# Kernel tuning notes

Measured on AMD Instinct MI355X. Metric: run time of the kernel, lower is better.

The kernel has to match this reference:

```python
import jax, jax.numpy as jnp
import numpy as np

B, C, D, H, W = 4, 128, 16, 16, 16
P = 64  # proj_dim (spatial branch is dead code in the original fusion; params omitted)


def setup_inputs() -> dict:
    key = jax.random.key(0)
    ks = jax.random.split(key, 10)
    lin = lambda k, o, i: 0.02 * jax.random.normal(k, (o, i), jnp.float32)
    return {
        "x": jax.random.normal(ks[0], (B, C, D, H, W), jnp.float32),
        "ln_g": jnp.ones((C,), jnp.float32),
        "ln_b": jnp.zeros((C,), jnp.float32),
        "Wq": lin(ks[1], C, C), "bq": jnp.zeros((C,), jnp.float32),
        "Wk": lin(ks[2], C, C), "bk": jnp.zeros((C,), jnp.float32),
        "Wvc": lin(ks[3], C, C), "bvc": jnp.zeros((C,), jnp.float32),
        "Wvch": lin(ks[4], C, C), "bvch": jnp.zeros((C,), jnp.float32),
        "Wconv": 0.02 * jax.random.normal(ks[5], (2, C, 3, 3, 3), jnp.float32),
        "bconv": jnp.zeros((2,), jnp.float32),
        "Wg": lin(ks[6], 3, C), "bg": jnp.zeros((3,), jnp.float32),
    }


def reference(x, ln_g, ln_b, Wq, bq, Wk, bk, Wvc, bvc, Wvch, bvch, Wconv, bconv, Wg, bg):
    b, c, d, h, w = x.shape
    n = d * h * w
    # LayerNorm over channels (permute to channels-last)
    xp = jnp.transpose(x, (0, 2, 3, 4, 1))                      # (B,D,H,W,C)
    mu = jnp.mean(xp, axis=-1, keepdims=True)
    var = jnp.mean((xp - mu) ** 2, axis=-1, keepdims=True)
    xn = (xp - mu) * jax.lax.rsqrt(var + 1e-5) * ln_g + ln_b     # (B,D,H,W,C)
    x_norm = jnp.transpose(xn, (0, 4, 1, 2, 3))                  # (B,C,D,H,W)
    # Causal Growth Field prediction: Conv3d C->2, k=3, SAME padding
    cgf = jax.lax.conv_general_dilated(
        x_norm, Wconv, (1, 1, 1), "SAME",
        dimension_numbers=("NCDHW", "OIDHW", "NCDHW")) + bconv[None, :, None, None, None]
    # Token sequence (B,N,C); same flattening order as x_norm.view(B,C,-1).transpose(1,2)
    xf = xn.reshape(b, n, c)
    q = jnp.einsum("bnc,oc->bno", xf, Wq) + bq
    k = jnp.einsum("bnc,oc->bno", xf, Wk) + bk
    # --- causal branch: full NxN attention ---
    vc = jnp.einsum("bnc,oc->bno", xf, Wvc) + bvc
    attn_causal = jax.nn.softmax(jnp.einsum("bnc,bmc->bnm", q, k) / (c ** 0.5), axis=-1)
    out_causal = jnp.einsum("bnm,bmc->bnc", attn_causal, vc)
    # --- channel branch: CxC attention ---
    vch = jnp.einsum("bnc,oc->bno", xf, Wvch) + bvch
    attn_channel = jax.nn.softmax(jnp.einsum("bnc,bnd->bcd", q, k) / (n ** 0.5), axis=-1)
    out_channel = jnp.einsum("bcd,bnd->bnc", attn_channel, vch)
    # --- gated fusion (original uses only weights 0 and 2; spatial branch is dead code) ---
    pooled = jnp.mean(x, axis=(2, 3, 4))                          # (B,C)
    weights = jax.nn.softmax(pooled @ Wg.T + bg, axis=-1)         # (B,3)
    fused = (weights[:, 0][:, None, None] * out_causal
             + weights[:, 2][:, None, None] * out_channel)        # (B,N,C)
    output = x + jnp.transpose(fused, (0, 2, 1)).reshape(b, c, d, h, w)
    return (output, cgf)
```

## Files before the change

kernel.cpp:

```cpp
#include <hip/hip_runtime.h>
#include <math.h>

#define CH   128
#define NSP  4096
#define BATCH 4
#define BIG  (BATCH*NSP*CH)
#define KCHUNKS 64
#define FKSPLIT 4
#define MB (1024*1024)

typedef short short8 __attribute__((ext_vector_type(8)));
typedef float floatx4 __attribute__((ext_vector_type(4)));

__device__ __forceinline__ unsigned short f2bu(float f) {
  union { float f; unsigned u; } v; v.f = f;
  unsigned r = v.u + 0x7fffu + ((v.u >> 16) & 1u);
  return (unsigned short)(r >> 16);
}
__device__ __forceinline__ float b2f(unsigned short h) {
  union { unsigned u; float f; } v; v.u = ((unsigned)h) << 16;
  return v.f;
}

__global__ __launch_bounds__(256) void ln_kernel(const float* __restrict__ x,
    const float* __restrict__ g, const float* __restrict__ bta,
    unsigned short* __restrict__ xfb) {
  __shared__ float tile[128][65];
  __shared__ float pS[4][64];
  __shared__ float pQ[4][64];
  __shared__ float mu_s[64], rs_s[64];
  int t = threadIdx.x;
  int b  = blockIdx.x >> 6;
  int n0 = (blockIdx.x & 63) << 6;
  for (int i = t; i < 8192; i += 256) {
    int c = i >> 6, n = i & 63;
    tile[c][n] = x[(size_t)(b*CH + c)*NSP + n0 + n];
  }
  __syncthreads();
  {
    int n = t & 63, part = t >> 6;
    float s = 0.f, qq = 0.f;
    for (int c = part; c < 128; c += 4) { float v = tile[c][n]; s += v; qq += v*v; }
    pS[part][n] = s; pQ[part][n] = qq;
  }
  __syncthreads();
  if (t < 64) {
    float s = pS[0][t] + pS[1][t] + pS[2][t] + pS[3][t];
    float qq = pQ[0][t] + pQ[1][t] + pQ[2][t] + pQ[3][t];
    float mu = s * (1.f/128.f);
    float var = qq * (1.f/128.f) - mu*mu;
    mu_s[t] = mu;
    rs_s[t] = rsqrtf(var + 1e-5f);
  }
  __syncthreads();
  for (int i = t; i < 8192; i += 256) {
    int n = i >> 7, c = i & 127;
    float v = (tile[c][n] - mu_s[n]) * rs_s[n] * g[c] + bta[c];
    xfb[(size_t)(b*NSP + n0 + n)*CH + c] = f2bu(v);
  }
}

__global__ __launch_bounds__(256) void pooled_kernel(const float* __restrict__ x,
                                                     float* __restrict__ pooled) {
  int bc = blockIdx.x; int t = threadIdx.x;
  const float4* p = (const float4*)(x + (size_t)bc*NSP);
  float s = 0.f;
  for (int i = t; i < 1024; i += 256) { float4 v = p[i]; s += v.x+v.y+v.z+v.w; }
  for (int off = 32; off; off >>= 1) s += __shfl_xor(s, off, 64);
  __shared__ float red[4];
  if ((t & 63) == 0) red[t >> 6] = s;
  __syncthreads();
  if (t == 0) pooled[bc] = (red[0]+red[1]+red[2]+red[3]) * (1.f/4096.f);
}

__global__ void gate_kernel(const float* __restrict__ pooled, const float* __restrict__ Wg,
                            const float* __restrict__ bg, float* __restrict__ wgt) {
  __shared__ float lg[4][3];
  int t = threadIdx.x;
  if (t < 12) {
    int b = t / 3, j = t % 3;
    float s = bg[j];
    const float* pr = pooled + b*CH;
    const float* wr = Wg + j*CH;
    for (int c = 0; c < CH; ++c) s += pr[c]*wr[c];
    lg[b][j] = s;
  }
  __syncthreads();
  if (t < 4) {
    float a = lg[t][0], b2 = lg[t][1], c = lg[t][2];
    float m = fmaxf(a, fmaxf(b2, c));
    float e0 = __expf(a-m), e1 = __expf(b2-m), e2 = __expf(c-m);
    float inv = 1.f/(e0+e1+e2);
    wgt[t*3+0] = e0*inv; wgt[t*3+1] = e1*inv; wgt[t*3+2] = e2*inv;
  }
}

__global__ __launch_bounds__(256) void conv_kernel(const unsigned short* __restrict__ xfb,
    const float* __restrict__ Wc, const float* __restrict__ bc_, float* __restrict__ cgf) {
  __shared__ float Wl[27*256];
  int t = threadIdx.x;
  for (int i = t; i < 6912; i += 256) {
    int tap = i >> 8;
    int rem = i & 255;
    int o = rem >> 7, c = rem & 127;
    Wl[i] = Wc[o*3456 + c*27 + tap];
  }
  __syncthreads();
  int cg = t & 15, spl = t >> 4;
  int sp = blockIdx.x*16 + spl;
  int b = sp >> 12, n = sp & 4095;
  int z = n >> 8, y = (n >> 4) & 15, xw = n & 15;
  const unsigned short* xb = xfb + (size_t)b*NSP*CH + cg*8;
  float a0 = 0.f, a1 = 0.f;
  for (int kd = 0; kd < 3; ++kd) {
    int zz = z + kd - 1; if ((unsigned)zz >= 16u) continue;
    for (int kh = 0; kh < 3; ++kh) {
      int yy = y + kh - 1; if ((unsigned)yy >= 16u) continue;
      #pragma unroll
      for (int kw = 0; kw < 3; ++kw) {
        int xx = xw + kw - 1; if ((unsigned)xx >= 16u) continue;
        int nn = (zz << 8) + (yy << 4) + xx;
        short8 xv = *(const short8*)(xb + (size_t)nn*CH);
        int tap = (kd*3 + kh)*3 + kw;
        const float* wbase = &Wl[tap*256 + cg*8];
        float4 w00 = *(const float4*)(wbase);
        float4 w01 = *(const float4*)(wbase + 4);
        float4 w10 = *(const float4*)(wbase + 128);
        float4 w11 = *(const float4*)(wbase + 132);
        float x0 = b2f((unsigned short)xv[0]), x1 = b2f((unsigned short)xv[1]);
        float x2 = b2f((unsigned short)xv[2]), x3 = b2f((unsigned short)xv[3]);
        float x4 = b2f((unsigned short)xv[4]), x5 = b2f((unsigned short)xv[5]);
        float x6 = b2f((unsigned short)xv[6]), x7 = b2f((unsigned short)xv[7]);
        a0 += x0*w00.x + x1*w00.y + x2*w00.z + x3*w00.w
            + x4*w01.x + x5*w01.y + x6*w01.z + x7*w01.w;
        a1 += x0*w10.x + x1*w10.y + x2*w10.z + x3*w10.w
            + x4*w11.x + x5*w11.y + x6*w11.z + x7*w11.w;
      }
    }
  }
  #pragma unroll
  for (int off = 1; off <= 8; off <<= 1) {
    a0 += __shfl_xor(a0, off, 64);
    a1 += __shfl_xor(a1, off, 64);
  }
  if (cg == 0) {
    cgf[b*8192 + n]        = a0 + bc_[0];
    cgf[b*8192 + 4096 + n] = a1 + bc_[1];
  }
}

__global__ __launch_bounds__(256) void wcast_kernel(const float* __restrict__ Wq,
    const float* __restrict__ Wk, const float* __restrict__ Wvc,
    const float* __restrict__ Wvch, unsigned short* __restrict__ Wb) {
  int idx = blockIdx.x*256 + threadIdx.x;
  int pj = idx >> 14, wi = idx & 16383;
  const float* src = (pj == 0) ? Wq : (pj == 1) ? Wk : (pj == 2) ? Wvc : Wvch;
  Wb[idx] = f2bu(src[wi]);
}

__global__ __launch_bounds__(256) void proj_mfma_kernel(
    const unsigned short* __restrict__ xfb, const unsigned short* __restrict__ Wb,
    const float* __restrict__ bq, const float* __restrict__ bk,
    const float* __restrict__ bvc, const float* __restrict__ bvch,
    unsigned short* __restrict__ q, unsigned short* __restrict__ k,
    unsigned short* __restrict__ vc, unsigned short* __restrict__ vch) {
  __shared__ __align__(16) unsigned short Ws[128][136];
  int t = threadIdx.x;
  int lane = t & 63, w = t >> 6;
  int id = lane & 15, quad = lane >> 4;
  int pj = blockIdx.y;
  int r0 = blockIdx.x*128 + w*32;

  const unsigned short* Wp = Wb + ((size_t)pj << 14);
  for (int i = t; i < 2048; i += 256) {
    int rr = i >> 4, c8 = (i & 15) << 3;
    *(short8*)&Ws[rr][c8] = *(const short8*)(Wp + rr*CH + c8);
  }
  short8 af[2][4];
  #pragma unroll
  for (int m = 0; m < 2; ++m)
    #pragma unroll
    for (int kc = 0; kc < 4; ++kc)
      af[m][kc] = *(const short8*)(xfb + (size_t)(r0 + m*16 + id)*CH + kc*32 + quad*8);
  __syncthreads();

  floatx4 acc[2][8];
  #pragma unroll
  for (int m = 0; m < 2; ++m)
    #pragma unroll
    for (int nt = 0; nt < 8; ++nt) acc[m][nt] = (floatx4){0.f,0.f,0.f,0.f};
  #pragma unroll
  for (int nt = 0; nt < 8; ++nt)
    #pragma unroll
    for (int kc = 0; kc < 4; ++kc) {
      short8 bf = *(const short8*)&Ws[nt*16 + id][kc*32 + quad*8];
      acc[0][nt] = __builtin_amdgcn_mfma_f32_16x16x32_bf16(af[0][kc], bf, acc[0][nt], 0, 0, 0);
      acc[1][nt] = __builtin_amdgcn_mfma_f32_16x16x32_bf16(af[1][kc], bf, acc[1][nt], 0, 0, 0);
    }

  const float* bias = (pj == 0) ? bq : (pj == 1) ? bk : (pj == 2) ? bvc : bvch;
  unsigned short* Y = (pj == 0) ? q : (pj == 1) ? k : (pj == 2) ? vc : vch;
  #pragma unroll
  for (int nt = 0; nt < 8; ++nt) {
    float bsv = bias[nt*16 + id];
    #pragma unroll
    for (int m = 0; m < 2; ++m)
      #pragma unroll
      for (int r = 0; r < 4; ++r) {
        int row = r0 + m*16 + quad*4 + r;
        Y[(size_t)row*CH + nt*16 + id] = f2bu(acc[m][nt][r] + bsv);
      }
  }
}

__global__ __launch_bounds__(256) void vtrans_kernel(const unsigned short* __restrict__ vc,
                                                     unsigned short* __restrict__ vct) {
  __shared__ unsigned short T[128][72];
  int t = threadIdx.x;
  int b = blockIdx.x >> 6, n0 = (blockIdx.x & 63) << 6;
  for (int i = t; i < 1024; i += 256) {
    int n = i >> 4, c0 = (i & 15) << 3;
    short8 v = *(const short8*)&vc[(size_t)(b*NSP + n0 + n)*CH + c0];
    #pragma unroll
    for (int j = 0; j < 8; ++j) T[c0+j][n] = (unsigned short)v[j];
  }
  __syncthreads();
  for (int i = t; i < 1024; i += 256) {
    int c = i >> 3, k8 = (i & 7) << 3;
    *(short8*)&vct[((size_t)b*CH + c)*NSP + n0 + k8] = *(short8*)&T[c][k8];
  }
}

__global__ __launch_bounds__(256) void chscore_kernel(const unsigned short* __restrict__ q,
    const unsigned short* __restrict__ k, float* __restrict__ Sp) {
  __shared__ unsigned short Qt[128][72];
  __shared__ unsigned short Kt[128][72];
  int t = threadIdx.x;
  int lane = t & 63, w = t >> 6;
  int id = lane & 15, quad = lane >> 4;
  int p = blockIdx.x;
  int b = blockIdx.y;
  const unsigned short* qb = q + (size_t)b*NSP*CH;
  const unsigned short* kb = k + (size_t)b*NSP*CH;
  int nbase = p*64;

  #pragma unroll
  for (int it = 0; it < 4; ++it) {
    int task = t + it*256;
    int c = task & 127, r0 = (task >> 7) << 3;
    short8 vq, vk;
    #pragma unroll
    for (int j = 0; j < 8; ++j) {
      size_t off = (size_t)(nbase + r0 + j)*CH + c;
      vq[j] = (short)qb[off];
      vk[j] = (short)kb[off];
    }
    *(short8*)&Qt[c][r0] = vq;
    *(short8*)&Kt[c][r0] = vk;
  }
  __syncthreads();

  floatx4 acc[2][8];
  #pragma unroll
  for (int mt = 0; mt < 2; ++mt)
    #pragma unroll
    for (int nt = 0; nt < 8; ++nt) acc[mt][nt] = (floatx4){0.f,0.f,0.f,0.f};
  #pragma unroll
  for (int kc = 0; kc < 2; ++kc) {
    short8 af0 = *(const short8*)&Qt[w*32 + id     ][kc*32 + quad*8];
    short8 af1 = *(const short8*)&Qt[w*32 + 16 + id][kc*32 + quad*8];
    #pragma unroll
    for (int nt = 0; nt < 8; ++nt) {
      short8 bf = *(const short8*)&Kt[nt*16 + id][kc*32 + quad*8];
      acc[0][nt] = __builtin_amdgcn_mfma_f32_16x16x32_bf16(af0, bf, acc[0][nt], 0, 0, 0);
      acc[1][nt] = __builtin_amdgcn_mfma_f32_16x16x32_bf16(af1, bf, acc[1][nt], 0, 0, 0);
    }
  }
  float* outp = Sp + ((size_t)(p*BATCH + b) << 14);
  #pragma unroll
  for (int mt = 0; mt < 2; ++mt)
    #pragma unroll
    for (int nt = 0; nt < 8; ++nt)
      #pragma unroll
      for (int r = 0; r < 4; ++r) {
        int c = w*32 + mt*16 + quad*4 + r;
        int d = nt*16 + id;
        outp[c*CH + d] = acc[mt][nt][r];
      }
}

__global__ __launch_bounds__(64) void chsoftmax_kernel(const float* __restrict__ Sp,
                                                       unsigned short* __restrict__ Sb) {
  int row = blockIdx.x;
  int b = row >> 7, c = row & 127;
  int t = threadIdx.x;
  float s0 = 0.f, s1 = 0.f;
  #pragma unroll 4
  for (int p = 0; p < KCHUNKS; ++p) {
    const float* r = Sp + (((size_t)(p*BATCH + b) << 7) + c)*CH;
    s0 += r[t]; s1 += r[t+64];
  }
  const float sc = 1.f/64.f;
  s0 *= sc; s1 *= sc;
  float m = fmaxf(s0, s1);
  for (int off = 32; off; off >>= 1) m = fmaxf(m, __shfl_xor(m, off, 64));
  float p0 = __expf(s0 - m), p1 = __expf(s1 - m);
  float s = p0 + p1;
  for (int off = 32; off; off >>= 1) s += __shfl_xor(s, off, 64);
  float inv = 1.f/s;
  unsigned short* r = Sb + (size_t)row*CH;
  r[t]    = f2bu(p0*inv);
  r[t+64] = f2bu(p1*inv);
}

__global__ __launch_bounds__(256) void chout_mfma_kernel(
    const unsigned short* __restrict__ vchb, const unsigned short* __restrict__ Sb,
    float* __restrict__ och) {
  __shared__ __align__(16) unsigned short As[128][136];
  int t = threadIdx.x;
  int lane = t & 63, w = t >> 6;
  int id = lane & 15, quad = lane >> 4;
  int b = blockIdx.x >> 5;
  int r0 = blockIdx.x*128 + w*32;

  const unsigned short* Sp = Sb + ((size_t)b << 14);
  for (int i = t; i < 2048; i += 256) {
    int rr = i >> 4, c8 = (i & 15) << 3;
    *(short8*)&As[rr][c8] = *(const short8*)(Sp + rr*CH + c8);
  }
  short8 af[2][4];
  #pragma unroll
  for (int m = 0; m < 2; ++m)
    #pragma unroll
    for (int kc = 0; kc < 4; ++kc)
      af[m][kc] = *(const short8*)(vchb + (size_t)(r0 + m*16 + id)*CH + kc*32 + quad*8);
  __syncthreads();

  floatx4 acc[2][8];
  #pragma unroll
  for (int m = 0; m < 2; ++m)
    #pragma unroll
    for (int nt = 0; nt < 8; ++nt) acc[m][nt] = (floatx4){0.f,0.f,0.f,0.f};
  #pragma unroll
  for (int nt = 0; nt < 8; ++nt)
    #pragma unroll
    for (int kc = 0; kc < 4; ++kc) {
      short8 bf = *(const short8*)&As[nt*16 + id][kc*32 + quad*8];
      acc[0][nt] = __builtin_amdgcn_mfma_f32_16x16x32_bf16(af[0][kc], bf, acc[0][nt], 0, 0, 0);
      acc[1][nt] = __builtin_amdgcn_mfma_f32_16x16x32_bf16(af[1][kc], bf, acc[1][nt], 0, 0, 0);
    }
  #pragma unroll
  for (int nt = 0; nt < 8; ++nt)
    #pragma unroll
    for (int m = 0; m < 2; ++m)
      #pragma unroll
      for (int r = 0; r < 4; ++r) {
        int row = r0 + m*16 + quad*4 + r;
        och[(size_t)row*CH + nt*16 + id] = acc[m][nt][r];
      }
}

__global__ __launch_bounds__(256) void flash_part_kernel(
    const unsigned short* __restrict__ Qg, const unsigned short* __restrict__ Kg,
    const unsigned short* __restrict__ Vtg,
    unsigned short* __restrict__ Opart, float* __restrict__ lpart) {
  __shared__ __align__(16) unsigned short Ks[64][136];
  __shared__ __align__(16) unsigned short Vt[128][72];
  __shared__ __align__(16) unsigned short Ps[4][32][68];
  int t = threadIdx.x;
  int lane = t & 63, w = t >> 6;
  int id = lane & 15, quad = lane >> 4;
  int blk = blockIdx.x;
  int x = blk & 7, y = blk >> 3;
  int tile = y & 31;
  int b = x >> 1;
  int ks = (x & 1) + ((y >> 5) << 1);
  int n0 = tile << 7;
  int r0 = n0 + w*32;

  const unsigned short* Qb = Qg  + (size_t)b*NSP*CH;
  const unsigned short* Kb = Kg  + (size_t)b*NSP*CH;
  const unsigned short* Vb = Vtg + (size_t)b*CH*NSP;

  int kr[4], kc8[4], vr[4], vn[4];
  #pragma unroll
  for (int it = 0; it < 4; ++it) {
    int task = t + it*256;
    kr[it] = task >> 4; kc8[it] = (task & 15) << 3;
    vr[it] = task >> 3; vn[it]  = (task & 7) << 3;
  }

  short8 qf[2][4];
  #pragma unroll
  for (int m = 0; m < 2; ++m)
    #pragma unroll
    for (int kc = 0; kc < 4; ++kc)
      qf[m][kc] = *(const short8*)(Qb + (size_t)(r0 + m*16 + id)*CH + kc*32 + quad*8);

  floatx4 O[2][8];
  #pragma unroll
  for (int m = 0; m < 2; ++m)
    #pragma unroll
    for (int ct = 0; ct < 8; ++ct) O[m][ct] = (floatx4){0.f,0.f,0.f,0.f};
  float lrun[2][4];
  #pragma unroll
  for (int m = 0; m < 2; ++m)
    #pragma unroll
    for (int r = 0; r < 4; ++r) lrun[m][r] = 0.f;

  const float scale = 0.08838834764831845f;

  short8 kreg[4], vreg[4];
  {
    int kbase = ks*1024;
    #pragma unroll
    for (int it = 0; it < 4; ++it) {
      kreg[it] = *(const short8*)(Kb + (size_t)(kbase + kr[it])*CH + kc8[it]);
      vreg[it] = *(const short8*)(Vb + (size_t)vr[it]*NSP + kbase + vn[it]);
    }
  }

  for (int kt = 0; kt < 16; ++kt) {
    __syncthreads();
    #pragma unroll
    for (int it = 0; it < 4; ++it) {
      *(short8*)&Ks[kr[it]][kc8[it]] = kreg[it];
      *(short8*)&Vt[vr[it]][vn[it]]  = vreg[it];
    }
    __syncthreads();
    if (kt < 15) {
      int kbase = ks*1024 + (kt+1)*64;
      #pragma unroll
      for (int it = 0; it < 4; ++it) {
        kreg[it] = *(const short8*)(Kb + (size_t)(kbase + kr[it])*CH + kc8[it]);
        vreg[it] = *(const short8*)(Vb + (size_t)vr[it]*NSP + kbase + vn[it]);
      }
    }

    floatx4 S[2][4];
    #pragma unroll
    for (int nt = 0; nt < 4; ++nt) {
      floatx4 a0 = (floatx4){0.f,0.f,0.f,0.f};
      floatx4 a1 = (floatx4){0.f,0.f,0.f,0.f};
      #pragma unroll
      for (int kc = 0; kc < 4; ++kc) {
        short8 kf = *(const short8*)&Ks[nt*16 + id][kc*32 + quad*8];
        a0 = __builtin_amdgcn_mfma_f32_16x16x32_bf16(qf[0][kc], kf, a0, 0, 0, 0);
        a1 = __builtin_amdgcn_mfma_f32_16x16x32_bf16(qf[1][kc], kf, a1, 0, 0, 0);
      }
      S[0][nt] = a0; S[1][nt] = a1;
    }
    #pragma unroll
    for (int m = 0; m < 2; ++m) {
      float rs[4] = {0.f,0.f,0.f,0.f};
      #pragma unroll
      for (int nt = 0; nt < 4; ++nt)
        #pragma unroll
        for (int r = 0; r < 4; ++r) {
          float p = __expf(S[m][nt][r] * scale);
          rs[r] += p;
          Ps[w][m*16 + quad*4 + r][nt*16 + id] = f2bu(p);
        }
      #pragma unroll
      for (int off = 1; off <= 8; off <<= 1)
        #pragma unroll
        for (int r = 0; r < 4; ++r) rs[r] += __shfl_xor(rs[r], off, 64);
      #pragma unroll
      for (int r = 0; r < 4; ++r) lrun[m][r] += rs[r];
    }
    #pragma unroll
    for (int nc = 0; nc < 2; ++nc) {
      short8 pf0 = *(const short8*)&Ps[w][id     ][nc*32 + quad*8];
      short8 pf1 = *(const short8*)&Ps[w][16 + id][nc*32 + quad*8];
      #pragma unroll
      for (int ct = 0; ct < 8; ++ct) {
        short8 vf = *(const short8*)&Vt[ct*16 + id][nc*32 + quad*8];
        O[0][ct] = __builtin_amdgcn_mfma_f32_16x16x32_bf16(pf0, vf, O[0][ct], 0, 0, 0);
        O[1][ct] = __builtin_amdgcn_mfma_f32_16x16x32_bf16(pf1, vf, O[1][ct], 0, 0, 0);
      }
    }
  }

  unsigned short* Op = Opart + (size_t)ks*BIG + (size_t)b*NSP*CH;
  #pragma unroll
  for (int m = 0; m < 2; ++m)
    #pragma unroll
    for (int ct = 0; ct < 8; ++ct)
      #pragma unroll
      for (int r = 0; r < 4; ++r) {
        int row = r0 + m*16 + quad*4 + r;
        Op[(size_t)row*CH + ct*16 + id] = f2bu(O[m][ct][r]);
      }
  if (id == 0) {
    float* lp = lpart + (size_t)ks*BATCH*NSP + (size_t)b*NSP;
    #pragma unroll
    for (int m = 0; m < 2; ++m)
      #pragma unroll
      for (int r = 0; r < 4; ++r)
        lp[r0 + m*16 + quad*4 + r] = lrun[m][r];
  }
}

__global__ __launch_bounds__(256) void fuse_kernel(const float* __restrict__ x,
    const unsigned short* __restrict__ Opart, const float* __restrict__ lpart,
    const float* __restrict__ och, const float* __restrict__ wgt,
    float* __restrict__ out) {
  __shared__ float T[128][65];
  __shared__ float linv[64];
  int t = threadIdx.x;
  int b  = blockIdx.x >> 6;
  int n0 = (blockIdx.x & 63) << 6;
  float w0 = wgt[b*3 + 0], w2 = wgt[b*3 + 2];
  if (t < 64) {
    float l = 0.f;
    #pragma unroll
    for (int p = 0; p < FKSPLIT; ++p)
      l += lpart[(size_t)p*BATCH*NSP + b*NSP + n0 + t];
    linv[t] = 1.f / l;
  }
  __syncthreads();
  const float* ochb = och + (size_t)(b*NSP + n0)*CH;
  for (int i = t; i < 8192; i += 256) {
    int n = i >> 7, c = i & 127;
    size_t oidx = (size_t)(b*NSP + n0 + n)*CH + c;
    float o = 0.f;
    #pragma unroll
    for (int p = 0; p < FKSPLIT; ++p) o += b2f(Opart[(size_t)p*BIG + oidx]);
    T[c][n] = w0*o*linv[n] + w2*ochb[(size_t)n*CH + c];
  }
  __syncthreads();
  for (int i = t; i < 8192; i += 256) {
    int c = i >> 6, n = i & 63;
    size_t idx = (size_t)(b*CH + c)*NSP + n0 + n;
    out[idx] = x[idx] + T[c][n];
  }
}

extern "C" void kernel_launch(void* const* d_in, const int* in_sizes, int n_in,
                              void* d_out, int out_size, void* d_ws, size_t ws_size,
                              hipStream_t stream) {
  (void)in_sizes; (void)n_in; (void)out_size; (void)ws_size;
  const float* x     = (const float*)d_in[0];
  const float* ln_g  = (const float*)d_in[1];
  const float* ln_b  = (const float*)d_in[2];
  const float* Wq    = (const float*)d_in[3];
  const float* bq    = (const float*)d_in[4];
  const float* Wk    = (const float*)d_in[5];
  const float* bk    = (const float*)d_in[6];
  const float* Wvc   = (const float*)d_in[7];
  const float* bvc   = (const float*)d_in[8];
  const float* Wvch  = (const float*)d_in[9];
  const float* bvch  = (const float*)d_in[10];
  const float* Wconv = (const float*)d_in[11];
  const float* bconv = (const float*)d_in[12];
  const float* Wg    = (const float*)d_in[13];
  const float* bg    = (const float*)d_in[14];

  float* out = (float*)d_out;
  float* cgf = out + (size_t)BIG;

  char* base = (char*)d_ws;
  float* och  = (float*)(base);
  unsigned short* Opart = (unsigned short*)(base + 8*(size_t)MB);
  float* Sp             = (float*)(base + 8*(size_t)MB);
  unsigned short* vcb   = (unsigned short*)(base + 24*(size_t)MB);
  float* lpart  = (float*)(base + 32*(size_t)MB);
  unsigned short* Schb = (unsigned short*)(base + 32*(size_t)MB + 512*1024);
  float* pooled = (float*)(base + 32*(size_t)MB + 768*1024);
  float* wgt    = pooled + BATCH*CH;
  unsigned short* qb   = (unsigned short*)(base + 33*(size_t)MB);
  unsigned short* kb   = (unsigned short*)(base + 37*(size_t)MB);
  unsigned short* vct  = (unsigned short*)(base + 41*(size_t)MB);
  unsigned short* vchb = (unsigned short*)(base + 45*(size_t)MB);
  unsigned short* Wb   = (unsigned short*)(base + 49*(size_t)MB);
  unsigned short* xfb  = (unsigned short*)(base + 49*(size_t)MB + 256*1024);

  ln_kernel     <<<256, 256, 0, stream>>>(x, ln_g, ln_b, xfb);
  pooled_kernel <<<512, 256, 0, stream>>>(x, pooled);
  gate_kernel   <<<1,   64,  0, stream>>>(pooled, Wg, bg, wgt);
  wcast_kernel  <<<256, 256, 0, stream>>>(Wq, Wk, Wvc, Wvch, Wb);
  conv_kernel   <<<1024, 256, 0, stream>>>(xfb, Wconv, bconv, cgf);
  proj_mfma_kernel<<<dim3(128,4), 256, 0, stream>>>(xfb, Wb, bq, bk, bvc, bvch,
                                                    qb, kb, vcb, vchb);
  vtrans_kernel <<<256, 256, 0, stream>>>(vcb, vct);
  chscore_kernel<<<dim3(KCHUNKS, BATCH), 256, 0, stream>>>(qb, kb, Sp);
  chsoftmax_kernel<<<512, 64, 0, stream>>>(Sp, Schb);
  chout_mfma_kernel<<<128, 256, 0, stream>>>(vchb, Schb, och);
  flash_part_kernel<<<512, 256, 0, stream>>>(qb, kb, vct, Opart, lpart);
  fuse_kernel   <<<256, 256, 0, stream>>>(x, Opart, lpart, och, wgt, out);
}
```

Baseline: 222.4 us.

## Fuse weight cast into projection, shrink channel-score partials, split flash keys six ways

Removes the separate weight-cast kernel by converting fp32 weights to bf16 while staging them into shared memory inside the projection kernel. The channel-score kernel now loops over four 64-row sub-chunks per block, cutting the partial count from 64 to 16 and so reducing partial-sum traffic for the softmax reduction. The flash attention key dimension is split six ways (uneven 11/10 tile chunks) across 768 blocks to raise occupancy, at the cost of more partials for the fuse step. Workspace offsets are moved to match.

Result: slower. 229.8 us (+3.3%).

```diff
diff --git a/kernel.cpp b/kernel.cpp
--- a/kernel.cpp
+++ b/kernel.cpp
@@ -5,8 +5,8 @@
 #define NSP  4096
 #define BATCH 4
 #define BIG  (BATCH*NSP*CH)
-#define KCHUNKS 64
-#define FKSPLIT 4
+#define KCHUNKS 16
+#define FKSPLIT 6
 #define MB (1024*1024)
 
 typedef short short8 __attribute__((ext_vector_type(8)));
@@ -149,17 +149,10 @@
   }
 }
 
-__global__ __launch_bounds__(256) void wcast_kernel(const float* __restrict__ Wq,
-    const float* __restrict__ Wk, const float* __restrict__ Wvc,
-    const float* __restrict__ Wvch, unsigned short* __restrict__ Wb) {
-  int idx = blockIdx.x*256 + threadIdx.x;
-  int pj = idx >> 14, wi = idx & 16383;
-  const float* src = (pj == 0) ? Wq : (pj == 1) ? Wk : (pj == 2) ? Wvc : Wvch;
-  Wb[idx] = f2bu(src[wi]);
-}
-
 __global__ __launch_bounds__(256) void proj_mfma_kernel(
-    const unsigned short* __restrict__ xfb, const unsigned short* __restrict__ Wb,
+    const unsigned short* __restrict__ xfb,
+    const float* __restrict__ Wq, const float* __restrict__ Wk,
+    const float* __restrict__ Wvc, const float* __restrict__ Wvch,
     const float* __restrict__ bq, const float* __restrict__ bk,
     const float* __restrict__ bvc, const float* __restrict__ bvch,
     unsigned short* __restrict__ q, unsigned short* __restrict__ k,
@@ -171,10 +164,14 @@
   int pj = blockIdx.y;
   int r0 = blockIdx.x*128 + w*32;
 
-  const unsigned short* Wp = Wb + ((size_t)pj << 14);
+  const float* Wp = (pj == 0) ? Wq : (pj == 1) ? Wk : (pj == 2) ? Wvc : Wvch;
   for (int i = t; i < 2048; i += 256) {
     int rr = i >> 4, c8 = (i & 15) << 3;
-    *(short8*)&Ws[rr][c8] = *(const short8*)(Wp + rr*CH + c8);
+    const float* src = Wp + rr*CH + c8;
+    short8 pk;
+    #pragma unroll
+    for (int j = 0; j < 8; ++j) pk[j] = (short)f2bu(src[j]);
+    *(short8*)&Ws[rr][c8] = pk;
   }
   short8 af[2][4];
   #pragma unroll
@@ -242,38 +239,41 @@
   int b = blockIdx.y;
   const unsigned short* qb = q + (size_t)b*NSP*CH;
   const unsigned short* kb = k + (size_t)b*NSP*CH;
-  int nbase = p*64;
-
-  #pragma unroll
-  for (int it = 0; it < 4; ++it) {
-    int task = t + it*256;
-    int c = task & 127, r0 = (task >> 7) << 3;
-    short8 vq, vk;
-    #pragma unroll
-    for (int j = 0; j < 8; ++j) {
-      size_t off = (size_t)(nbase + r0 + j)*CH + c;
-      vq[j] = (short)qb[off];
-      vk[j] = (short)kb[off];
-    }
-    *(short8*)&Qt[c][r0] = vq;
-    *(short8*)&Kt[c][r0] = vk;
-  }
-  __syncthreads();
 
   floatx4 acc[2][8];
   #pragma unroll
   for (int mt = 0; mt < 2; ++mt)
     #pragma unroll
     for (int nt = 0; nt < 8; ++nt) acc[mt][nt] = (floatx4){0.f,0.f,0.f,0.f};
-  #pragma unroll
-  for (int kc = 0; kc < 2; ++kc) {
-    short8 af0 = *(const short8*)&Qt[w*32 + id     ][kc*32 + quad*8];
-    short8 af1 = *(const short8*)&Qt[w*32 + 16 + id][kc*32 + quad*8];
-    #pragma unroll
-    for (int nt = 0; nt < 8; ++nt) {
-      short8 bf = *(const short8*)&Kt[nt*16 + id][kc*32 + quad*8];
-      acc[0][nt] = __builtin_amdgcn_mfma_f32_16x16x32_bf16(af0, bf, acc[0][nt], 0, 0, 0);
-      acc[1][nt] = __builtin_amdgcn_mfma_f32_16x16x32_bf16(af1, bf, acc[1][nt], 0, 0, 0);
+
+  for (int s = 0; s < 4; ++s) {
+    int nbase = p*256 + s*64;
+    __syncthreads();
+    #pragma unroll
+    for (int it = 0; it < 4; ++it) {
+      int task = t + it*256;
+      int c = task & 127, r0 = (task >> 7) << 3;
+      short8 vq, vk;
+      #pragma unroll
+      for (int j = 0; j < 8; ++j) {
+        size_t off = (size_t)(nbase + r0 + j)*CH + c;
+        vq[j] = (short)qb[off];
+        vk[j] = (short)kb[off];
+      }
+      *(short8*)&Qt[c][r0] = vq;
+      *(short8*)&Kt[c][r0] = vk;
+    }
+    __syncthreads();
+    #pragma unroll
+    for (int kc = 0; kc < 2; ++kc) {
+      short8 af0 = *(const short8*)&Qt[w*32 + id     ][kc*32 + quad*8];
+      short8 af1 = *(const short8*)&Qt[w*32 + 16 + id][kc*32 + quad*8];
+      #pragma unroll
+      for (int nt = 0; nt < 8; ++nt) {
+        short8 bf = *(const short8*)&Kt[nt*16 + id][kc*32 + quad*8];
+        acc[0][nt] = __builtin_amdgcn_mfma_f32_16x16x32_bf16(af0, bf, acc[0][nt], 0, 0, 0);
+        acc[1][nt] = __builtin_amdgcn_mfma_f32_16x16x32_bf16(af1, bf, acc[1][nt], 0, 0, 0);
+      }
     }
   }
   float* outp = Sp + ((size_t)(p*BATCH + b) << 14);
@@ -373,8 +373,11 @@
   int blk = blockIdx.x;
   int x = blk & 7, y = blk >> 3;
   int tile = y & 31;
-  int b = x >> 1;
-  int ks = (x & 1) + ((y >> 5) << 1);
+  int cid = x*3 + (y >> 5);
+  int b = cid & 3;
+  int ks = cid >> 2;
+  int ksoff = (ks < 4) ? ks*11 : 44 + (ks - 4)*10;
+  int kcnt  = (ks < 4) ? 11 : 10;
   int n0 = tile << 7;
   int r0 = n0 + w*32;
 
@@ -412,7 +415,7 @@
 
   short8 kreg[4], vreg[4];
   {
-    int kbase = ks*1024;
+    int kbase = ksoff*64;
     #pragma unroll
     for (int it = 0; it < 4; ++it) {
       kreg[it] = *(const short8*)(Kb + (size_t)(kbase + kr[it])*CH + kc8[it]);
@@ -420,7 +423,7 @@
     }
   }
 
-  for (int kt = 0; kt < 16; ++kt) {
+  for (int kt = 0; kt < kcnt; ++kt) {
     __syncthreads();
     #pragma unroll
     for (int it = 0; it < 4; ++it) {
@@ -428,8 +431,8 @@
       *(short8*)&Vt[vr[it]][vn[it]]  = vreg[it];
     }
     __syncthreads();
-    if (kt < 15) {
-      int kbase = ks*1024 + (kt+1)*64;
+    if (kt < kcnt - 1) {
+      int kbase = (ksoff + kt + 1)*64;
       #pragma unroll
       for (int it = 0; it < 4; ++it) {
         kreg[it] = *(const short8*)(Kb + (size_t)(kbase + kr[it])*CH + kc8[it]);
@@ -563,7 +566,7 @@
   float* och  = (float*)(base);
   unsigned short* Opart = (unsigned short*)(base + 8*(size_t)MB);
   float* Sp             = (float*)(base + 8*(size_t)MB);
-  unsigned short* vcb   = (unsigned short*)(base + 24*(size_t)MB);
+  unsigned short* vcb   = (unsigned short*)(base + 12*(size_t)MB);
   float* lpart  = (float*)(base + 32*(size_t)MB);
   unsigned short* Schb = (unsigned short*)(base + 32*(size_t)MB + 512*1024);
   float* pooled = (float*)(base + 32*(size_t)MB + 768*1024);
@@ -572,20 +575,19 @@
   unsigned short* kb   = (unsigned short*)(base + 37*(size_t)MB);
   unsigned short* vct  = (unsigned short*)(base + 41*(size_t)MB);
   unsigned short* vchb = (unsigned short*)(base + 45*(size_t)MB);
-  unsigned short* Wb   = (unsigned short*)(base + 49*(size_t)MB);
-  unsigned short* xfb  = (unsigned short*)(base + 49*(size_t)MB + 256*1024);
+  unsigned short* xfb  = (unsigned short*)(base + 49*(size_t)MB);
 
   ln_kernel     <<<256, 256, 0, stream>>>(x, ln_g, ln_b, xfb);
   pooled_kernel <<<512, 256, 0, stream>>>(x, pooled);
   gate_kernel   <<<1,   64,  0, stream>>>(pooled, Wg, bg, wgt);
-  wcast_kernel  <<<256, 256, 0, stream>>>(Wq, Wk, Wvc, Wvch, Wb);
   conv_kernel   <<<1024, 256, 0, stream>>>(xfb, Wconv, bconv, cgf);
-  proj_mfma_kernel<<<dim3(128,4), 256, 0, stream>>>(xfb, Wb, bq, bk, bvc, bvch,
+  proj_mfma_kernel<<<dim3(128,4), 256, 0, stream>>>(xfb, Wq, Wk, Wvc, Wvch,
+                                                    bq, bk, bvc, bvch,
                                                     qb, kb, vcb, vchb);
   vtrans_kernel <<<256, 256, 0, stream>>>(vcb, vct);
   chscore_kernel<<<dim3(KCHUNKS, BATCH), 256, 0, stream>>>(qb, kb, Sp);
   chsoftmax_kernel<<<512, 64, 0, stream>>>(Sp, Schb);
   chout_mfma_kernel<<<128, 256, 0, stream>>>(vchb, Schb, och);
-  flash_part_kernel<<<512, 256, 0, stream>>>(qb, kb, vct, Opart, lpart);
+  flash_part_kernel<<<768, 256, 0, stream>>>(qb, kb, vct, Opart, lpart);
   fuse_kernel   <<<256, 256, 0, stream>>>(x, Opart, lpart, och, wgt, out);
 }
```
